# Optimization experiments

Hardware: AMD Instinct MI355X
Metric: run time of the kernel (lower is better)

Reference implementation:

```python
import jax, jax.numpy as jnp
import numpy as np

D = 768      # activation_dim
F = 16384    # dict_size
K = 64       # top-k
B = 4096     # batch of activation vectors


def setup_inputs() -> dict:
    key = jax.random.key(0)
    k1, k2, k3 = jax.random.split(key, 3)
    x = jax.random.normal(k1, (B, D), dtype=jnp.float32)
    W_enc = jax.random.normal(k2, (F, D), dtype=jnp.float32) * 0.02
    b_enc = jnp.zeros((F,), dtype=jnp.float32)
    W_dec = jax.random.normal(k3, (D, F), dtype=jnp.float32)
    # decoder columns normalized to unit norm (set_decoder_norm_to_unit_norm)
    eps = jnp.finfo(jnp.float32).eps
    W_dec = W_dec / (jnp.linalg.norm(W_dec, axis=0, keepdims=True) + eps)
    b_dec = jnp.zeros((D,), dtype=jnp.float32)
    return {"x": x, "W_enc": W_enc, "b_enc": b_enc, "W_dec": W_dec, "b_dec": b_dec}


def reference(x, W_enc, b_enc, W_dec, b_dec):
    # encode: pre_activation_BF = encoder(x - b_dec)
    pre_BF = jnp.einsum('bd,fd->bf', x - b_dec, W_enc) + b_enc
    # top-k selection along feature dim
    vals_BK, idx_BK = jax.lax.top_k(pre_BF, K)
    # scatter top-k values into sparse code buffer [B, F]
    rows = jnp.arange(pre_BF.shape[0])[:, None]
    f_BF = jnp.zeros_like(pre_BF).at[rows, idx_BK].set(vals_BK)
    # decode: x_hat = decoder(f) + b_dec
    x_hat_BD = jnp.einsum('bf,df->bd', f_BF, W_dec) + b_dec
    return x_hat_BD
```

## Files before the change

kernel.cpp:

```cpp
#include <hip/hip_runtime.h>
#include <cstdint>
#include <cstddef>

#define Dd 768
#define Ff 16384
#define Bb 4096
#define Kk 64
#define NCAND 128
#define BINS 512
#define MARGIN 0.04f

typedef __bf16 bf16x8 __attribute__((ext_vector_type(8)));
typedef float  f32x4  __attribute__((ext_vector_type(4)));
typedef unsigned short u16x8 __attribute__((ext_vector_type(8)));

__device__ __forceinline__ unsigned short f2bf(float f) {
    union { float f; unsigned u; } a; a.f = f;
    unsigned r = a.u + 0x7fffu + ((a.u >> 16) & 1u);
    return (unsigned short)(r >> 16);
}
__device__ __forceinline__ float bf2f(unsigned short h) {
    union { float f; unsigned u; } a; a.u = ((unsigned)h) << 16;
    return a.f;
}
__device__ __forceinline__ float f_lo(unsigned u) {
    union { float f; unsigned u; } a; a.u = u << 16; return a.f;
}
__device__ __forceinline__ float f_hi(unsigned u) {
    union { float f; unsigned u; } a; a.u = u & 0xffff0000u; return a.f;
}

#define GLDS16(g, l) __builtin_amdgcn_global_load_lds( \
    (const __attribute__((address_space(1))) void*)(g), \
    (__attribute__((address_space(3))) void*)(l), 16, 0, 0)

__global__ __launch_bounds__(256) void conv_x(
    const float* __restrict__ x, const float* __restrict__ bdec,
    unsigned short* __restrict__ Xb)
{
    const int i = blockIdx.x * 256 + threadIdx.x;
    const int col = i % Dd;
    Xb[i] = f2bf(x[i] - bdec[col]);
}

__global__ __launch_bounds__(256) void conv_w(
    const float* __restrict__ Wenc, unsigned short* __restrict__ Wb)
{
    const int i = blockIdx.x * 256 + threadIdx.x;
    Wb[i] = f2bf(Wenc[i]);
}

__global__ __launch_bounds__(256) void sae_gemm(
    const unsigned short* __restrict__ Xb,
    const unsigned short* __restrict__ Wb,
    const float* __restrict__ benc,
    unsigned short* __restrict__ pre)
{
    __shared__ __align__(16) unsigned short As[128 * 32];
    __shared__ __align__(16) unsigned short Bs[128 * 32];

    const int tid  = threadIdx.x;
    const int lane = tid & 63;
    const int w    = tid >> 6;
    const int wm   = w >> 1, wn = w & 1;
    const int m0   = blockIdx.y * 128;
    const int n0   = blockIdx.x * 128;

    const int e = tid * 8;
    const unsigned short* gA0 = Xb + (size_t)(m0 + (e >> 5)) * Dd + (e & 31);
    const unsigned short* gA1 = Xb + (size_t)(m0 + 64 + (e >> 5)) * Dd + (e & 31);
    const unsigned short* gB0 = Wb + (size_t)(n0 + (e >> 5)) * Dd + (e & 31);
    const unsigned short* gB1 = Wb + (size_t)(n0 + 64 + (e >> 5)) * Dd + (e & 31);
    unsigned short* lA0 = &As[w * 512];
    unsigned short* lA1 = &As[2048 + w * 512];
    unsigned short* lB0 = &Bs[w * 512];
    unsigned short* lB1 = &Bs[2048 + w * 512];

    f32x4 acc[4][4];
    #pragma unroll
    for (int i = 0; i < 4; ++i)
        #pragma unroll
        for (int j = 0; j < 4; ++j) acc[i][j] = 0;

    const int aro = (wm * 64 + (lane & 15)) * 32 + (lane >> 4) * 8;
    const int bro = (wn * 64 + (lane & 15)) * 32 + (lane >> 4) * 8;

    for (int k0 = 0; k0 < Dd; k0 += 32) {
        __syncthreads();
        GLDS16(gA0 + k0, lA0);
        GLDS16(gA1 + k0, lA1);
        GLDS16(gB0 + k0, lB0);
        GLDS16(gB1 + k0, lB1);
        __syncthreads();
        bf16x8 af[4], bfr[4];
        #pragma unroll
        for (int mi = 0; mi < 4; ++mi) af[mi]  = *(const bf16x8*)&As[aro + mi * 512];
        #pragma unroll
        for (int ni = 0; ni < 4; ++ni) bfr[ni] = *(const bf16x8*)&Bs[bro + ni * 512];
        #pragma unroll
        for (int mi = 0; mi < 4; ++mi)
            #pragma unroll
            for (int ni = 0; ni < 4; ++ni)
                acc[mi][ni] = __builtin_amdgcn_mfma_f32_16x16x32_bf16(
                    af[mi], bfr[ni], acc[mi][ni], 0, 0, 0);
    }

    const int cl = lane & 15;
    const int rl = (lane >> 4) * 4;
    #pragma unroll
    for (int ni = 0; ni < 4; ++ni) {
        const int ccol = n0 + wn * 64 + ni * 16 + cl;
        const float bia = benc[ccol];
        #pragma unroll
        for (int mi = 0; mi < 4; ++mi) {
            const int row = m0 + wm * 64 + mi * 16 + rl;
            #pragma unroll
            for (int j = 0; j < 4; ++j)
                pre[(size_t)(row + j) * Ff + ccol] = f2bf(acc[mi][ni][j] + bia);
        }
    }
}

__global__ __launch_bounds__(256) void sae_select(
    const unsigned short* __restrict__ pre,
    int* __restrict__ ci, int* __restrict__ ccount)
{
    __shared__ unsigned hist[2][BINS];
    __shared__ float tauS[2];
    __shared__ int lcnt[2];

    const int tid = threadIdx.x;
    const int r   = tid >> 7;
    const int l   = tid & 127;
    const int rg  = blockIdx.x * 2 + r;

    for (int i = tid; i < 2 * BINS; i += 256) ((unsigned*)hist)[i] = 0;
    if (tid < 2) lcnt[tid] = 0;
    __syncthreads();

    const u16x8* rp = (const u16x8*)(pre + (size_t)rg * Ff);
    for (int j = 0; j < 16; ++j) {
        const u16x8 v8 = rp[j * 128 + l];
        #pragma unroll
        for (int c = 0; c < 8; ++c) {
            const float v = bf2f(v8[c]);
            if (v >= 0.0f) {
                const int b = min((int)(v * 128.0f), BINS - 1);
                atomicAdd(&hist[r][b], 1u);
            }
        }
    }
    __syncthreads();

    if (l == 0) {
        unsigned acc = 0; float tv = -1.0e30f;
        for (int j = BINS - 1; j >= 0; --j) {
            acc += hist[r][j];
            if (acc >= (unsigned)Kk) { tv = (float)j * 0.0078125f; break; }
        }
        tauS[r] = tv;
    }
    __syncthreads();

    const float thr = tauS[r] - MARGIN;
    for (int j = 0; j < 16; ++j) {
        const u16x8 v8 = rp[j * 128 + l];
        #pragma unroll
        for (int c = 0; c < 8; ++c) {
            const float v = bf2f(v8[c]);
            if (v >= thr) {
                const int p = atomicAdd(&lcnt[r], 1);
                if (p < NCAND) ci[(size_t)rg * NCAND + p] = j * 1024 + l * 8 + c;
            }
        }
    }
    __syncthreads();
    if (l == 0) ccount[rg] = min(lcnt[r], NCAND);
}

__global__ __launch_bounds__(256) void sae_rescore(
    const float* __restrict__ x, const float* __restrict__ Wenc,
    const float* __restrict__ benc, const float* __restrict__ bdec,
    const int* __restrict__ ci, const int* __restrict__ ccount,
    float* __restrict__ ovals, int* __restrict__ oidx)
{
    __shared__ float  xr[Dd];
    __shared__ int    cis[NCAND];
    __shared__ double es[NCAND];
    __shared__ int    cnt;

    const int r = blockIdx.x, tid = threadIdx.x;
    const int lane = tid & 63, w = tid >> 6;

    xr[tid]       = x[(size_t)r * Dd + tid]       - bdec[tid];
    xr[tid + 256] = x[(size_t)r * Dd + tid + 256] - bdec[tid + 256];
    xr[tid + 512] = x[(size_t)r * Dd + tid + 512] - bdec[tid + 512];
    if (tid == 0) cnt = ccount[r];
    if (tid < NCAND) cis[tid] = ci[(size_t)r * NCAND + tid];
    if (tid < Kk) { ovals[(size_t)r * Kk + tid] = 0.0f; oidx[(size_t)r * Kk + tid] = 0; }
    __syncthreads();

    for (int c = w; c < NCAND; c += 4) {
        double e = -1.0e300;
        if (c < cnt) {
            const int f = cis[c];
            const float* wrow = Wenc + (size_t)f * Dd;
            double a = 0.0;
            #pragma unroll
            for (int j = 0; j < Dd / 64; ++j)
                a = fma((double)wrow[j * 64 + lane], (double)xr[j * 64 + lane], a);
            #pragma unroll
            for (int off = 32; off > 0; off >>= 1)
                a += __shfl_xor(a, off);
            e = a + (double)benc[f];
        }
        if (lane == 0) es[c] = e;
    }
    __syncthreads();

    if (tid < NCAND) {
        const double e = es[tid];
        int rk = 0;
        for (int j = 0; j < NCAND; ++j) {
            const double ej = es[j];
            rk += (ej > e) || (ej == e && j < tid);
        }
        if (tid < cnt && rk < Kk) {
            ovals[(size_t)r * Kk + rk] = (float)e;
            oidx [(size_t)r * Kk + rk] = cis[tid];
        }
    }
}

__global__ __launch_bounds__(256) void sae_transpose(
    const float* __restrict__ Wd, unsigned short* __restrict__ WdT)
{
    __shared__ float tile[32][33];
    const int f0 = blockIdx.x * 32;
    const int d0 = blockIdx.y * 32;
    const int tx = threadIdx.x, ty = threadIdx.y;
    #pragma unroll
    for (int k = 0; k < 4; ++k)
        tile[ty + 8 * k][tx] = Wd[(size_t)(d0 + ty + 8 * k) * Ff + f0 + tx];
    __syncthreads();
    #pragma unroll
    for (int k = 0; k < 4; ++k)
        WdT[(size_t)(f0 + ty + 8 * k) * Dd + d0 + tx] = f2bf(tile[tx][ty + 8 * k]);
}

__global__ __launch_bounds__(192) void sae_decode(
    const unsigned short* __restrict__ WdT, const float* __restrict__ vals,
    const int* __restrict__ idx, const float* __restrict__ bdec,
    float* __restrict__ out)
{
    __shared__ float sv[Kk];
    __shared__ int   si[Kk];
    const int b = blockIdx.x, tid = threadIdx.x;
    if (tid < Kk) { sv[tid] = vals[(size_t)b * Kk + tid]; si[tid] = idx[(size_t)b * Kk + tid]; }
    __syncthreads();
    const int d0 = tid * 4;
    float a0 = bdec[d0], a1 = bdec[d0 + 1], a2 = bdec[d0 + 2], a3 = bdec[d0 + 3];
    for (int k = 0; k < Kk; ++k) {
        const float v = sv[k];
        const uint2 p = *(const uint2*)(WdT + (size_t)si[k] * Dd + d0);
        a0 = fmaf(v, f_lo(p.x), a0);
        a1 = fmaf(v, f_hi(p.x), a1);
        a2 = fmaf(v, f_lo(p.y), a2);
        a3 = fmaf(v, f_hi(p.y), a3);
    }
    float4 o4 = make_float4(a0, a1, a2, a3);
    *(float4*)(out + (size_t)b * Dd + d0) = o4;
}

extern "C" void kernel_launch(void* const* d_in, const int* in_sizes, int n_in,
                              void* d_out, int out_size, void* d_ws, size_t ws_size,
                              hipStream_t stream) {
    const float* x    = (const float*)d_in[0];
    const float* Wenc = (const float*)d_in[1];
    const float* benc = (const float*)d_in[2];
    const float* Wdec = (const float*)d_in[3];
    const float* bdec = (const float*)d_in[4];
    float* out = (float*)d_out;

    char* ws = (char*)d_ws;
    size_t o = 0;
    unsigned short* pre  = (unsigned short*)(ws + o); o += (size_t)Bb * Ff * 2;
    unsigned short* Xb   = (unsigned short*)(ws + o); o += (size_t)Bb * Dd * 2;
    unsigned short* Wb   = (unsigned short*)(ws + o); o += (size_t)Ff * Dd * 2;
    unsigned short* WdT  = (unsigned short*)(ws + o); o += (size_t)Ff * Dd * 2;
    int*            cib  = (int*)(ws + o);            o += (size_t)Bb * NCAND * 4;
    int*            ccnt = (int*)(ws + o);            o += (size_t)Bb * 4;
    float*          vals = (float*)(ws + o);          o += (size_t)Bb * Kk * 4;
    int*            idxb = (int*)(ws + o);

    conv_x<<<(Bb * Dd) / 256, 256, 0, stream>>>(x, bdec, Xb);
    conv_w<<<(Ff * Dd) / 256, 256, 0, stream>>>(Wenc, Wb);
    sae_gemm<<<dim3(Ff / 128, Bb / 128), 256, 0, stream>>>(Xb, Wb, benc, pre);
    sae_select<<<Bb / 2, 256, 0, stream>>>(pre, cib, ccnt);
    sae_rescore<<<Bb, 256, 0, stream>>>(x, Wenc, benc, bdec, cib, ccnt, vals, idxb);
    sae_transpose<<<dim3(Ff / 32, Dd / 32), dim3(32, 8), 0, stream>>>(Wdec, WdT);
    sae_decode<<<Bb, 192, 0, stream>>>(WdT, vals, idxb, bdec, out);
}
```

Baseline: 553.8 us.

## Rewrite encoder GEMM with 256x256 tiles, double-buffered LDS and swizzled reads

The encoder GEMM moves from 128x128 tiles with 4 waves and two barriers per K step to 256x256 tiles with 8 waves. It double-buffers 64-wide K slices in LDS with asynchronous global-to-LDS loads issued one phase ahead, and uses rotated LDS read offsets to avoid bank conflicts. It also adds an XCD-aware block index remap and raises MFMA priority with setprio. The aim is to hide global load latency behind MFMA work and raise arithmetic intensity, at the cost of 128KB of LDS per block, higher register pressure, and hand-tuned vmcnt waits that are fragile.

```diff
diff --git a/kernel.cpp b/kernel.cpp
--- a/kernel.cpp
+++ b/kernel.cpp
@@ -50,75 +50,132 @@
     Wb[i] = f2bf(Wenc[i]);
 }
 
-__global__ __launch_bounds__(256) void sae_gemm(
+__global__ __launch_bounds__(512, 2) void sae_gemm(
     const unsigned short* __restrict__ Xb,
     const unsigned short* __restrict__ Wb,
     const float* __restrict__ benc,
     unsigned short* __restrict__ pre)
 {
-    __shared__ __align__(16) unsigned short As[128 * 32];
-    __shared__ __align__(16) unsigned short Bs[128 * 32];
+    __shared__ __align__(16) unsigned short As[32768];
+    __shared__ __align__(16) unsigned short Bs[32768];
 
     const int tid  = threadIdx.x;
     const int lane = tid & 63;
     const int w    = tid >> 6;
-    const int wm   = w >> 1, wn = w & 1;
-    const int m0   = blockIdx.y * 128;
-    const int n0   = blockIdx.x * 128;
-
-    const int e = tid * 8;
-    const unsigned short* gA0 = Xb + (size_t)(m0 + (e >> 5)) * Dd + (e & 31);
-    const unsigned short* gA1 = Xb + (size_t)(m0 + 64 + (e >> 5)) * Dd + (e & 31);
-    const unsigned short* gB0 = Wb + (size_t)(n0 + (e >> 5)) * Dd + (e & 31);
-    const unsigned short* gB1 = Wb + (size_t)(n0 + 64 + (e >> 5)) * Dd + (e & 31);
-    unsigned short* lA0 = &As[w * 512];
-    unsigned short* lA1 = &As[2048 + w * 512];
-    unsigned short* lB0 = &Bs[w * 512];
-    unsigned short* lB1 = &Bs[2048 + w * 512];
-
-    f32x4 acc[4][4];
+    const int wm   = w >> 2, wn = w & 3;
+
+    const int bid = blockIdx.x;
+    const int wg  = (bid & 7) * 128 + (bid >> 3);
+    const int n0  = (wg & 63) * 256;
+    const int m0  = (wg >> 6) * 256;
+
+    const int r0 = tid >> 2,           r1 = (512 + tid) >> 2;
+    const int q0 = (tid - (tid >> 3)) & 3;
+    const int q1 = ((512 + tid) - ((512 + tid) >> 3)) & 3;
+    const unsigned short* aS0 = Xb + (size_t)(m0 + r0) * Dd + q0 * 8;
+    const unsigned short* aS1 = Xb + (size_t)(m0 + r1) * Dd + q1 * 8;
+    const unsigned short* bS0 = Wb + (size_t)(n0 + r0) * Dd + q0 * 8;
+    const unsigned short* bS1 = Wb + (size_t)(n0 + r1) * Dd + q1 * 8;
+    unsigned short* lA = As + w * 512;
+    unsigned short* lB = Bs + w * 512;
+
+    const int rl  = lane & 15;
+    const int rot = ((lane >> 4) + (rl >> 1)) & 3;
+    const unsigned asO = (unsigned)(unsigned long long)
+        (__attribute__((address_space(3))) unsigned short*)&As[0];
+    const unsigned bsO = (unsigned)(unsigned long long)
+        (__attribute__((address_space(3))) unsigned short*)&Bs[0];
+    const unsigned aRd = asO + (unsigned)((wm * 128 + rl) * 64 + rot * 16);
+    const unsigned bRd = bsO + (unsigned)((wn * 64 + rl) * 64 + rot * 16);
+
+    f32x4 acc[8][4];
     #pragma unroll
-    for (int i = 0; i < 4; ++i)
+    for (int i = 0; i < 8; ++i)
         #pragma unroll
         for (int j = 0; j < 4; ++j) acc[i][j] = 0;
 
-    const int aro = (wm * 64 + (lane & 15)) * 32 + (lane >> 4) * 8;
-    const int bro = (wn * 64 + (lane & 15)) * 32 + (lane >> 4) * 8;
-
-    for (int k0 = 0; k0 < Dd; k0 += 32) {
-        __syncthreads();
-        GLDS16(gA0 + k0, lA0);
-        GLDS16(gA1 + k0, lA1);
-        GLDS16(gB0 + k0, lB0);
-        GLDS16(gB1 + k0, lB1);
-        __syncthreads();
-        bf16x8 af[4], bfr[4];
-        #pragma unroll
-        for (int mi = 0; mi < 4; ++mi) af[mi]  = *(const bf16x8*)&As[aro + mi * 512];
-        #pragma unroll
-        for (int ni = 0; ni < 4; ++ni) bfr[ni] = *(const bf16x8*)&Bs[bro + ni * 512];
-        #pragma unroll
-        for (int mi = 0; mi < 4; ++mi)
-            #pragma unroll
-            for (int ni = 0; ni < 4; ++ni)
-                acc[mi][ni] = __builtin_amdgcn_mfma_f32_16x16x32_bf16(
-                    af[mi], bfr[ni], acc[mi][ni], 0, 0, 0);
+#define DSR(D, A) asm volatile("ds_read_b128 %0, %1" : "=v"(D) : "v"(A))
+#define STG1(MS0, MS1, LDSB, TILE, KH, BUF) {                                 \
+    GLDS16(MS0 + (TILE) * 64 + (KH) * 32,                                     \
+           LDSB + (BUF) * 16384 + (KH) * 8192);                               \
+    GLDS16(MS1 + (TILE) * 64 + (KH) * 32,                                     \
+           LDSB + (BUF) * 16384 + (KH) * 8192 + 4096); }
+#define STAGE_G(TILE, KH, BUF) { STG1(aS0, aS1, lA, TILE, KH, BUF);           \
+                                 STG1(bS0, bS1, lB, TILE, KH, BUF); }
+#define VM8 asm volatile("s_waitcnt vmcnt(8)" ::: "memory")
+
+#define MF1(H, MI, NI) acc[(H)*4+(MI)][(NI)] =                                \
+    __builtin_amdgcn_mfma_f32_16x16x32_bf16(                                  \
+        __builtin_bit_cast(bf16x8, af[(MI)]),                                 \
+        __builtin_bit_cast(bf16x8, bfr[(NI)]), acc[(H)*4+(MI)][(NI)], 0, 0, 0)
+#define MFQ(H)                                                                \
+    MF1(H,0,0); MF1(H,0,1); MF1(H,0,2); MF1(H,0,3);                           \
+    MF1(H,1,0); MF1(H,1,1); MF1(H,1,2); MF1(H,1,3);                           \
+    MF1(H,2,0); MF1(H,2,1); MF1(H,2,2); MF1(H,2,3);                           \
+    MF1(H,3,0); MF1(H,3,1); MF1(H,3,2); MF1(H,3,3)
+
+#define PH(BUF, KH, H, STAGE_STMT, VM_STMT) {                                 \
+    f32x4 af[4];                                                              \
+    const unsigned ab = aRd + (BUF)*32768 + (KH)*16384 + (H)*4096;            \
+    DSR(af[0], ab);        DSR(af[1], ab + 1024);                             \
+    DSR(af[2], ab + 2048); DSR(af[3], ab + 3072);                             \
+    if ((H) == 0) {                                                           \
+        const unsigned bb = bRd + (BUF)*32768 + (KH)*16384;                   \
+        DSR(bfr[0], bb);        DSR(bfr[1], bb + 1024);                       \
+        DSR(bfr[2], bb + 2048); DSR(bfr[3], bb + 3072);                       \
+    }                                                                         \
+    STAGE_STMT;                                                               \
+    __builtin_amdgcn_s_barrier();                                             \
+    asm volatile("s_waitcnt lgkmcnt(0)" ::: "memory");                        \
+    __builtin_amdgcn_sched_barrier(0);                                        \
+    __builtin_amdgcn_s_setprio(1);                                            \
+    MFQ(H);                                                                   \
+    __builtin_amdgcn_s_setprio(0);                                            \
+    VM_STMT;                                                                  \
+    __builtin_amdgcn_s_barrier(); }
+
+    STAGE_G(0, 0, 0);
+    STAGE_G(0, 1, 0);
+    STAGE_G(1, 0, 1);
+    asm volatile("s_waitcnt vmcnt(8)" ::: "memory");
+    __builtin_amdgcn_s_barrier();
+
+    f32x4 bfr[4];
+    for (int i = 0; i < 6; ++i) {
+        const int t1 = 2 * i + 1, t2 = 2 * i + 2, t3 = 2 * i + 3;
+        PH(0, 0, 0, STAGE_G(t1, 1, 1), (void)0);
+        PH(0, 0, 1, (void)0,           VM8);
+        PH(0, 1, 0, STAGE_G(t2, 0, 0), (void)0);
+        PH(0, 1, 1, (void)0,           VM8);
+        PH(1, 0, 0, STAGE_G(t2, 1, 0), (void)0);
+        PH(1, 0, 1, (void)0,           VM8);
+        PH(1, 1, 0, STAGE_G(t3, 0, 1), (void)0);
+        PH(1, 1, 1, (void)0,           VM8);
     }
 
     const int cl = lane & 15;
-    const int rl = (lane >> 4) * 4;
+    const int rb = (lane >> 4) * 4;
     #pragma unroll
     for (int ni = 0; ni < 4; ++ni) {
         const int ccol = n0 + wn * 64 + ni * 16 + cl;
         const float bia = benc[ccol];
         #pragma unroll
-        for (int mi = 0; mi < 4; ++mi) {
-            const int row = m0 + wm * 64 + mi * 16 + rl;
+        for (int mi = 0; mi < 8; ++mi) {
+            const int row = m0 + wm * 128 + mi * 16 + rb;
             #pragma unroll
             for (int j = 0; j < 4; ++j)
                 pre[(size_t)(row + j) * Ff + ccol] = f2bf(acc[mi][ni][j] + bia);
         }
     }
+    asm volatile("s_waitcnt vmcnt(0)" ::: "memory");
+
+#undef DSR
+#undef STG1
+#undef STAGE_G
+#undef VM8
+#undef MF1
+#undef MFQ
+#undef PH
 }
 
 __global__ __launch_bounds__(256) void sae_select(
@@ -295,7 +352,7 @@
 
     conv_x<<<(Bb * Dd) / 256, 256, 0, stream>>>(x, bdec, Xb);
     conv_w<<<(Ff * Dd) / 256, 256, 0, stream>>>(Wenc, Wb);
-    sae_gemm<<<dim3(Ff / 128, Bb / 128), 256, 0, stream>>>(Xb, Wb, benc, pre);
+    sae_gemm<<<(Bb / 256) * (Ff / 256), 512, 0, stream>>>(Xb, Wb, benc, pre);
     sae_select<<<Bb / 2, 256, 0, stream>>>(pre, cib, ccnt);
     sae_rescore<<<Bb, 256, 0, stream>>>(x, Wenc, benc, bdec, cib, ccnt, vals, idxb);
     sae_transpose<<<dim3(Ff / 32, Dd / 32), dim3(32, 8), 0, stream>>>(Wdec, WdT);
```

Result: no change. 553.6 us (-0.0%).
